# Kernel optimization log

Measured on AMD Instinct MI355X. Metric: run time of the kernel, lower is better.

Reference implementation:

```python
import jax, jax.numpy as jnp
import numpy as np

N_HEADS = 4

def log_cosh(x):
    # numerically stable log(cosh(x)) = |x| + log1p(exp(-2|x|)) - log(2)
    ax = jnp.abs(x)
    return ax + jnp.log1p(jnp.exp(-2.0 * ax)) - jnp.log(2.0)

def setup_inputs() -> dict:
    key = jax.random.key(0)
    ks = jax.random.split(key, 7)
    B, I, A, E, H = 4, 2048, 2048, 256, N_HEADS
    return {
        "query": jax.random.normal(ks[0], (B, I, E), dtype=jnp.float32),
        "key": jax.random.normal(ks[1], (B, A, E), dtype=jnp.float32),
        "value": jax.random.normal(ks[2], (B, A, E), dtype=jnp.float32),
        "distances": jax.random.uniform(ks[3], (B, I, A), dtype=jnp.float32),
        "in_proj_w": jax.random.normal(ks[4], (3 * E, E), dtype=jnp.float32) * 0.05,
        "out_proj_w": jax.random.normal(ks[5], (E, E), dtype=jnp.float32) * 0.05,
        "mass_w": jax.random.normal(ks[6], (H, E), dtype=jnp.float32) * 0.05,
    }

def reference(query, key, value, distances, in_proj_w, out_proj_w, mass_w):
    B, I, E = query.shape
    A = key.shape[1]
    H = N_HEADS
    D = E // H
    # distance-decay additive bias: mass is (B, A, H), nonnegative via log_cosh
    mass = log_cosh(key @ mass_w.T)                       # (B, A, H)
    bias = jnp.einsum('bah,bia->bhia', -mass, distances)  # (B, H, I, A)
    # nn.MultiheadAttention (bias=False) projections
    wq, wk, wv = jnp.split(in_proj_w, 3, axis=0)          # each (E, E)
    q = (query @ wq.T).reshape(B, I, H, D).transpose(0, 2, 1, 3)  # (B,H,I,D)
    k = (key @ wk.T).reshape(B, A, H, D).transpose(0, 2, 1, 3)    # (B,H,A,D)
    v = (value @ wv.T).reshape(B, A, H, D).transpose(0, 2, 1, 3)  # (B,H,A,D)
    scale = 1.0 / jnp.sqrt(jnp.asarray(D, dtype=q.dtype))
    scores = jnp.einsum('bhid,bhad->bhia', q, k) * scale + bias
    attn = jax.nn.softmax(scores, axis=-1)
    o = jnp.einsum('bhia,bhad->bhid', attn, v)            # (B,H,I,D)
    o = o.transpose(0, 2, 1, 3).reshape(B, I, E)
    return o @ out_proj_w.T
```

## Files before the change

kernel.cpp:

```cpp
#include <hip/hip_runtime.h>
#include <hip/hip_bf16.h>
#include <math.h>

#define BB 4
#define II 2048
#define AA 2048
#define EE 256
#define HH 4

#define LOG2E 1.4426950408889634f
#define SCL   (0.125f * LOG2E)

typedef __bf16 bf16_t;
typedef bf16_t bf16x8 __attribute__((ext_vector_type(8)));
typedef bf16_t bf16x4 __attribute__((ext_vector_type(4)));
typedef float  f32x4  __attribute__((ext_vector_type(4)));

static __device__ __forceinline__ f32x4 mfma16(bf16x8 a, bf16x8 b, f32x4 c) {
    return __builtin_amdgcn_mfma_f32_16x16x32_bf16(a, b, c, 0, 0, 0);
}

static __device__ __forceinline__ void glds16(const bf16_t* g, const bf16_t* l) {
    __builtin_amdgcn_global_load_lds(
        (const __attribute__((address_space(1))) void*)g,
        (__attribute__((address_space(3))) void*)l, 16, 0, 0);
}

static __device__ __forceinline__ void proj_body(
    const float* __restrict__ Aop, const float* __restrict__ Bop,
    bf16_t* __restrict__ Cout, int m0, int n0, int TRANS, float cscale,
    bf16_t (*sA)[72], bf16_t (*sB)[72])
{
    const int t = threadIdx.x;
    const int w = t >> 6, l = t & 63, g = l >> 4, q = l & 15;
    const int wm = w >> 1, wn = w & 1;
    const int r = t >> 2, s = t & 3;

    f32x4 acc[2][2] = {};

    for (int kt = 0; kt < 4; ++kt) {
        {
            const float* ga = Aop + (size_t)(m0 + r) * EE + kt * 64 + s * 16;
            float tmp[16];
            *(f32x4*)&tmp[0]  = *(const f32x4*)(ga + 0);
            *(f32x4*)&tmp[4]  = *(const f32x4*)(ga + 4);
            *(f32x4*)&tmp[8]  = *(const f32x4*)(ga + 8);
            *(f32x4*)&tmp[12] = *(const f32x4*)(ga + 12);
            bf16x8 w0, w1;
            #pragma unroll
            for (int i = 0; i < 8; ++i) { w0[i] = (bf16_t)tmp[i]; w1[i] = (bf16_t)tmp[8 + i]; }
            *(bf16x8*)&sA[r][s * 16]     = w0;
            *(bf16x8*)&sA[r][s * 16 + 8] = w1;
        }
        {
            const float* gb = Bop + (size_t)(n0 + r) * EE + kt * 64 + s * 16;
            float tmp[16];
            *(f32x4*)&tmp[0]  = *(const f32x4*)(gb + 0);
            *(f32x4*)&tmp[4]  = *(const f32x4*)(gb + 4);
            *(f32x4*)&tmp[8]  = *(const f32x4*)(gb + 8);
            *(f32x4*)&tmp[12] = *(const f32x4*)(gb + 12);
            bf16x8 w0, w1;
            #pragma unroll
            for (int i = 0; i < 8; ++i) { w0[i] = (bf16_t)tmp[i]; w1[i] = (bf16_t)tmp[8 + i]; }
            *(bf16x8*)&sB[r][s * 16]     = w0;
            *(bf16x8*)&sB[r][s * 16 + 8] = w1;
        }
        __syncthreads();
        #pragma unroll
        for (int ks = 0; ks < 2; ++ks) {
            bf16x8 aA[2], aB[2];
            #pragma unroll
            for (int f = 0; f < 2; ++f) {
                aA[f] = *(const bf16x8*)&sA[wm * 32 + f * 16 + q][ks * 32 + g * 8];
                aB[f] = *(const bf16x8*)&sB[wn * 32 + f * 16 + q][ks * 32 + g * 8];
            }
            #pragma unroll
            for (int fm = 0; fm < 2; ++fm)
            #pragma unroll
            for (int fn = 0; fn < 2; ++fn)
                acc[fm][fn] = mfma16(aA[fm], aB[fn], acc[fm][fn]);
        }
        __syncthreads();
    }
    #pragma unroll
    for (int fm = 0; fm < 2; ++fm)
    #pragma unroll
    for (int fn = 0; fn < 2; ++fn)
    #pragma unroll
    for (int j = 0; j < 4; ++j) {
        const int m = m0 + wm * 32 + fm * 16 + g * 4 + j;
        const int n = n0 + wn * 32 + fn * 16 + q;
        const bf16_t v = (bf16_t)(acc[fm][fn][j] * cscale);
        if (TRANS == 0) {
            Cout[(size_t)m * EE + n] = v;
        } else {
            const int bb = n >> 11, a = n & (AA - 1);
            const int a6 = a & 63;
            const int p6 = (a6 & 32) | ((a6 & 12) << 1) | ((a6 & 16) >> 2) | (a6 & 3);
            Cout[(size_t)bb * (AA * EE) + (size_t)(a >> 6) * (EE * 64) + m * 64 + p6] = v;
        }
    }
}

__global__ __launch_bounds__(256) void fused_pre(
    const float* __restrict__ query, const float* __restrict__ key,
    const float* __restrict__ value, const float* __restrict__ in_w,
    const float* __restrict__ mass_w,
    bf16_t* __restrict__ Qp, bf16_t* __restrict__ Kp, bf16_t* __restrict__ Vt,
    float* __restrict__ massT)
{
    __shared__ __align__(16) bf16_t sA[64][72];
    __shared__ __align__(16) bf16_t sB[64][72];
    const int z = blockIdx.z;
    if (z == 0) {
        proj_body(query, in_w, Qp, blockIdx.x * 64, blockIdx.y * 64, 0, SCL, sA, sB);
    } else if (z == 1) {
        proj_body(key, in_w + 65536, Kp, blockIdx.x * 64, blockIdx.y * 64, 0, 1.0f, sA, sB);
    } else if (z == 2) {
        proj_body(in_w + 131072, value, Vt, blockIdx.y * 64, blockIdx.x * 64, 1, 1.0f, sA, sB);
    } else {
        const int w = threadIdx.x >> 6, l = threadIdx.x & 63;
        const int p = blockIdx.y * 128 + blockIdx.x;
        const int row0 = p * 16 + w * 4;
        f32x4 mw[HH];
        #pragma unroll
        for (int hh = 0; hh < HH; ++hh)
            mw[hh] = *(const f32x4*)(mass_w + hh * EE + l * 4);
        #pragma unroll
        for (int rr = 0; rr < 4; ++rr) {
            const int row = row0 + rr;
            f32x4 kv = *(const f32x4*)(key + (size_t)row * EE + l * 4);
            f32x4 sd;
            #pragma unroll
            for (int hh = 0; hh < HH; ++hh)
                sd[hh] = kv[0]*mw[hh][0] + kv[1]*mw[hh][1] + kv[2]*mw[hh][2] + kv[3]*mw[hh][3];
            #pragma unroll
            for (int off = 32; off >= 1; off >>= 1) {
                #pragma unroll
                for (int hh = 0; hh < HH; ++hh) sd[hh] += __shfl_xor(sd[hh], off, 64);
            }
            if (l == 0) {
                const int bb = row >> 11, a = row & (AA - 1);
                #pragma unroll
                for (int hh = 0; hh < HH; ++hh) {
                    float ax = fabsf(sd[hh]);
                    massT[((size_t)bb * HH + hh) * AA + a] =
                        (ax + log1pf(__expf(-2.0f * ax)) - 0.693147180559945f) * LOG2E;
                }
            }
        }
    }
}

__global__ __launch_bounds__(256) void out_gemm(
    const bf16_t* __restrict__ Aop, const float* __restrict__ Bop,
    float* __restrict__ Cout)
{
    __shared__ __align__(16) bf16_t sA[64][72];
    __shared__ __align__(16) bf16_t sB[64][72];
    const int t = threadIdx.x;
    const int w = t >> 6, l = t & 63, g = l >> 4, q = l & 15;
    const int wm = w >> 1, wn = w & 1;
    const int m0 = blockIdx.x * 64, n0 = blockIdx.y * 64;
    const int r = t >> 2, s = t & 3;

    f32x4 acc[2][2] = {};

    for (int kt = 0; kt < 4; ++kt) {
        {
            const bf16_t* ga = Aop + (size_t)(m0 + r) * EE + kt * 64 + s * 16;
            *(bf16x8*)&sA[r][s * 16]     = *(const bf16x8*)(ga);
            *(bf16x8*)&sA[r][s * 16 + 8] = *(const bf16x8*)(ga + 8);
        }
        {
            const float* gb = Bop + (size_t)(n0 + r) * EE + kt * 64 + s * 16;
            float tmp[16];
            *(f32x4*)&tmp[0]  = *(const f32x4*)(gb + 0);
            *(f32x4*)&tmp[4]  = *(const f32x4*)(gb + 4);
            *(f32x4*)&tmp[8]  = *(const f32x4*)(gb + 8);
            *(f32x4*)&tmp[12] = *(const f32x4*)(gb + 12);
            bf16x8 w0, w1;
            #pragma unroll
            for (int i = 0; i < 8; ++i) { w0[i] = (bf16_t)tmp[i]; w1[i] = (bf16_t)tmp[8 + i]; }
            *(bf16x8*)&sB[r][s * 16]     = w0;
            *(bf16x8*)&sB[r][s * 16 + 8] = w1;
        }
        __syncthreads();
        #pragma unroll
        for (int ks = 0; ks < 2; ++ks) {
            bf16x8 aA[2], aB[2];
            #pragma unroll
            for (int f = 0; f < 2; ++f) {
                aA[f] = *(const bf16x8*)&sA[wm * 32 + f * 16 + q][ks * 32 + g * 8];
                aB[f] = *(const bf16x8*)&sB[wn * 32 + f * 16 + q][ks * 32 + g * 8];
            }
            #pragma unroll
            for (int fm = 0; fm < 2; ++fm)
            #pragma unroll
            for (int fn = 0; fn < 2; ++fn)
                acc[fm][fn] = mfma16(aA[fm], aB[fn], acc[fm][fn]);
        }
        __syncthreads();
    }
    #pragma unroll
    for (int fm = 0; fm < 2; ++fm)
    #pragma unroll
    for (int fn = 0; fn < 2; ++fn)
    #pragma unroll
    for (int j = 0; j < 4; ++j) {
        const int m = m0 + wm * 32 + fm * 16 + g * 4 + j;
        const int n = n0 + wn * 32 + fn * 16 + q;
        Cout[(size_t)m * EE + n] = acc[fm][fn][j];
    }
}

__global__ __launch_bounds__(512, 4) void attn_kernel(
    const bf16_t* __restrict__ Qp, const bf16_t* __restrict__ Kp,
    const bf16_t* __restrict__ Vt, const float* __restrict__ massT,
    const float* __restrict__ dist, bf16_t* __restrict__ Obuf)
{
    __shared__ __align__(16) bf16_t sK[2][2][4096];
    __shared__ __align__(16) bf16_t sV[2][2][4096];
    __shared__ __align__(16) float  sM[2048];

    const int t = threadIdx.x;
    const int wv = t >> 6, l = t & 63, g = l >> 4, q = l & 15;
    const int s = wv >> 2, rg = wv & 3;
    const int h = blockIdx.y, b = blockIdx.z;
    const int i0 = blockIdx.x * 64;

    *(f32x4*)&sM[t * 4] = *(const f32x4*)(massT + ((size_t)b * HH + h) * AA + t * 4);

    bf16x8 qf[2];
    #pragma unroll
    for (int ks = 0; ks < 2; ++ks)
        qf[ks] = *(const bf16x8*)(Qp + (size_t)(b * II + i0 + rg * 16 + q) * EE
                                     + h * 64 + ks * 32 + g * 8);

    const int u0 = rg * 2;
    const int drow0 = u0 * 8 + (l >> 3);
    const int cs = (l & 7) ^ (drow0 & 7);

    const bf16_t* pkg = Kp + ((size_t)b * AA + s * 64 + drow0) * EE + h * 64 + cs * 8;
    const bf16_t* pvg = Vt + (size_t)b * (AA * EE) + (size_t)s * (EE * 64)
                           + (size_t)(h * 64 + drow0) * 64 + cs * 8;
    const float*  pdg = dist + ((size_t)b * II + i0 + rg * 16 + q) * AA + s * 64 + g * 4;

    auto stage = [&](int kb) {
        #pragma unroll
        for (int u = 0; u < 2; ++u) {
            glds16(pkg + u * (8 * EE), &sK[s][kb][(u0 + u) * 512]);
            glds16(pvg + u * (8 * 64), &sV[s][kb][(u0 + u) * 512]);
        }
    };

    f32x4 rd[2][4];

    stage(0);
    pkg += 128 * EE; pvg += 2 * (EE * 64);
    #pragma unroll
    for (int fa = 0; fa < 4; ++fa) rd[0][fa] = *(const f32x4*)(pdg + fa * 16);
    pdg += 128;
    __syncthreads();

    f32x4 oacc[4] = {};
    f32x4 lacc = {};
    bf16x8 vone;
    #pragma unroll
    for (int j = 0; j < 8; ++j) vone[j] = (bf16_t)1.0f;

    int ma = s * 64;

    #pragma unroll 2
    for (int k = 0; k < 16; ++k) {
        const int kb = k & 1;
        if (k < 15) {
            stage(kb ^ 1);
            pkg += 128 * EE; pvg += 2 * (EE * 64);
            #pragma unroll
            for (int fa = 0; fa < 4; ++fa)
                rd[(k + 1) & 1][fa] = *(const f32x4*)(pdg + fa * 16);
            pdg += 128;
        }

        f32x4 st[4] = {};
        __builtin_amdgcn_s_setprio(1);
        #pragma unroll
        for (int fa = 0; fa < 4; ++fa) {
            const int row = fa * 16 + q;
            #pragma unroll
            for (int ks = 0; ks < 2; ++ks) {
                bf16x8 ak = *(const bf16x8*)&sK[s][kb][row * 64 + (((ks * 4 + g) ^ (row & 7)) * 8)];
                st[fa] = mfma16(ak, qf[ks], st[fa]);
            }
        }
        __builtin_amdgcn_s_setprio(0);

        #pragma unroll
        for (int fa = 0; fa < 4; ++fa) {
            f32x4 ms = *(const f32x4*)&sM[ma + fa * 16 + g * 4];
            #pragma unroll
            for (int j = 0; j < 4; ++j)
                st[fa][j] = exp2f(fmaf(-ms[j], rd[kb][fa][j], st[fa][j]));
        }
        ma += 128;

        bf16x8 pa[2];
        #pragma unroll
        for (int ka = 0; ka < 2; ++ka)
        #pragma unroll
        for (int j = 0; j < 8; ++j)
            pa[ka][j] = (bf16_t)st[2 * ka + (j >> 2)][j & 3];

        __builtin_amdgcn_s_setprio(1);
        #pragma unroll
        for (int ka = 0; ka < 2; ++ka) {
            #pragma unroll
            for (int fd = 0; fd < 4; ++fd) {
                const int row = fd * 16 + q;
                bf16x8 bv = *(const bf16x8*)&sV[s][kb][row * 64 + (((ka * 4 + g) ^ (row & 7)) * 8)];
                oacc[fd] = mfma16(pa[ka], bv, oacc[fd]);
            }
            lacc = mfma16(pa[ka], vone, lacc);
        }
        __builtin_amdgcn_s_setprio(0);

        __syncthreads();
    }

    float* cb = (float*)&sK[0][0][0];
    if (s == 1) {
        float* p = cb + (rg * 64 + l) * 21;
        *(f32x4*)(p) = lacc;
        #pragma unroll
        for (int fd = 0; fd < 4; ++fd) *(f32x4*)(p + 4 + fd * 4) = oacc[fd];
    }
    __syncthreads();
    if (s == 0) {
        const float* p = cb + (rg * 64 + l) * 21;
        const f32x4 lB = *(const f32x4*)(p);
        f32x4 inv;
        #pragma unroll
        for (int j = 0; j < 4; ++j) inv[j] = 1.0f / (lacc[j] + lB[j]);
        #pragma unroll
        for (int fd = 0; fd < 4; ++fd) {
            const f32x4 ob = *(const f32x4*)(p + 4 + fd * 4);
            #pragma unroll
            for (int j = 0; j < 4; ++j) {
                const float o = (oacc[fd][j] + ob[j]) * inv[j];
                Obuf[(size_t)(b * II + i0 + rg * 16 + g * 4 + j) * EE
                     + h * 64 + fd * 16 + q] = (bf16_t)o;
            }
        }
    }
}

extern "C" void kernel_launch(void* const* d_in, const int* in_sizes, int n_in,
                              void* d_out, int out_size, void* d_ws, size_t ws_size,
                              hipStream_t stream)
{
    const float* query  = (const float*)d_in[0];
    const float* key    = (const float*)d_in[1];
    const float* value  = (const float*)d_in[2];
    const float* dist   = (const float*)d_in[3];
    const float* in_w   = (const float*)d_in[4];
    const float* out_w  = (const float*)d_in[5];
    const float* mass_w = (const float*)d_in[6];
    float* out = (float*)d_out;

    char* ws = (char*)d_ws;
    bf16_t* Qp    = (bf16_t*)(ws);
    bf16_t* Kp    = (bf16_t*)(ws + 1 * 4194304);
    bf16_t* Vt    = (bf16_t*)(ws + 2 * 4194304);
    bf16_t* Obuf  = (bf16_t*)(ws + 3 * 4194304);
    float*  massT = (float*) (ws + 4 * 4194304);

    fused_pre<<<dim3(128, 4, 4), dim3(256), 0, stream>>>(
        query, key, value, in_w, mass_w, Qp, Kp, Vt, massT);
    attn_kernel<<<dim3(32, 4, 4), dim3(512), 0, stream>>>(Qp, Kp, Vt, massT, dist, Obuf);
    out_gemm<<<dim3(128, 4), dim3(256), 0, stream>>>(Obuf, out_w, out);
}
```

Before: 80.55 us.

## Split attention key range across four wave groups with two query fragments per wave

Changes the wave decomposition from two key-splits by four row groups into four key-splits by two row groups. Each wave now holds two 16-row query fragments and processes a 32-key slice per step, so each K/V fragment read from shared memory feeds two MFMAs and LDS read traffic per MFMA drops. The V tile layout changes to 32-wide rows without the XOR swizzle. The final reduction now merges partial sums from three wave groups through shared memory. The cost is more accumulator registers per wave and a larger cross-wave combine step.

```diff
diff --git a/kernel.cpp b/kernel.cpp
--- a/kernel.cpp
+++ b/kernel.cpp
@@ -219,57 +219,63 @@
     const bf16_t* __restrict__ Vt, const float* __restrict__ massT,
     const float* __restrict__ dist, bf16_t* __restrict__ Obuf)
 {
-    __shared__ __align__(16) bf16_t sK[2][2][4096];
-    __shared__ __align__(16) bf16_t sV[2][2][4096];
+    __shared__ __align__(16) bf16_t sK[4][2][32 * 64];
+    __shared__ __align__(16) bf16_t sV[4][2][64 * 32];
     __shared__ __align__(16) float  sM[2048];
 
     const int t = threadIdx.x;
     const int wv = t >> 6, l = t & 63, g = l >> 4, q = l & 15;
-    const int s = wv >> 2, rg = wv & 3;
+    const int s = wv >> 1, rg = wv & 1;
     const int h = blockIdx.y, b = blockIdx.z;
     const int i0 = blockIdx.x * 64;
 
     *(f32x4*)&sM[t * 4] = *(const f32x4*)(massT + ((size_t)b * HH + h) * AA + t * 4);
 
-    bf16x8 qf[2];
+    bf16x8 qf[2][2];
+    #pragma unroll
+    for (int fq = 0; fq < 2; ++fq)
     #pragma unroll
     for (int ks = 0; ks < 2; ++ks)
-        qf[ks] = *(const bf16x8*)(Qp + (size_t)(b * II + i0 + rg * 16 + q) * EE
-                                     + h * 64 + ks * 32 + g * 8);
-
-    const int u0 = rg * 2;
-    const int drow0 = u0 * 8 + (l >> 3);
-    const int cs = (l & 7) ^ (drow0 & 7);
-
-    const bf16_t* pkg = Kp + ((size_t)b * AA + s * 64 + drow0) * EE + h * 64 + cs * 8;
-    const bf16_t* pvg = Vt + (size_t)b * (AA * EE) + (size_t)s * (EE * 64)
-                           + (size_t)(h * 64 + drow0) * 64 + cs * 8;
-    const float*  pdg = dist + ((size_t)b * II + i0 + rg * 16 + q) * AA + s * 64 + g * 4;
+        qf[fq][ks] = *(const bf16x8*)(Qp + (size_t)(b * II + i0 + rg * 32 + fq * 16 + q) * EE
+                                         + h * 64 + ks * 32 + g * 8);
+
+    const int kcs = (l & 7) ^ (l >> 3);
+    const bf16_t* pkg = Kp + ((size_t)b * AA + s * 32 + rg * 16 + (l >> 3)) * EE
+                           + h * 64 + kcs * 8;
+
+    const bf16_t* pvg = Vt + (size_t)b * (AA * EE) + (size_t)(s >> 1) * (EE * 64)
+                           + (size_t)(h * 64 + rg * 32 + (l >> 2)) * 64
+                           + (s & 1) * 32 + (l & 3) * 8;
+
+    const float* pdg0 = dist + ((size_t)(b * II + i0 + rg * 32 + q)) * AA + s * 32 + g * 4;
+    const float* pdg1 = pdg0 + (size_t)16 * AA;
 
     auto stage = [&](int kb) {
-        #pragma unroll
-        for (int u = 0; u < 2; ++u) {
-            glds16(pkg + u * (8 * EE), &sK[s][kb][(u0 + u) * 512]);
-            glds16(pvg + u * (8 * 64), &sV[s][kb][(u0 + u) * 512]);
-        }
+        glds16(pkg,            &sK[s][kb][(rg * 16) * 64]);
+        glds16(pkg + 8 * EE,   &sK[s][kb][(rg * 16 + 8) * 64]);
+        glds16(pvg,            &sV[s][kb][(rg * 32) * 32]);
+        glds16(pvg + 16 * 64,  &sV[s][kb][(rg * 32 + 16) * 32]);
     };
 
-    f32x4 rd[2][4];
+    f32x4 rd[2][2][2];
 
     stage(0);
     pkg += 128 * EE; pvg += 2 * (EE * 64);
     #pragma unroll
-    for (int fa = 0; fa < 4; ++fa) rd[0][fa] = *(const f32x4*)(pdg + fa * 16);
-    pdg += 128;
+    for (int fa = 0; fa < 2; ++fa) {
+        rd[0][0][fa] = *(const f32x4*)(pdg0 + fa * 16);
+        rd[0][1][fa] = *(const f32x4*)(pdg1 + fa * 16);
+    }
+    pdg0 += 128; pdg1 += 128;
     __syncthreads();
 
-    f32x4 oacc[4] = {};
-    f32x4 lacc = {};
+    f32x4 oacc[2][4] = {};
+    f32x4 lacc[2] = {};
     bf16x8 vone;
     #pragma unroll
     for (int j = 0; j < 8; ++j) vone[j] = (bf16_t)1.0f;
 
-    int ma = s * 64;
+    int ma = s * 32;
 
     #pragma unroll 2
     for (int k = 0; k < 16; ++k) {
@@ -278,78 +284,100 @@
             stage(kb ^ 1);
             pkg += 128 * EE; pvg += 2 * (EE * 64);
             #pragma unroll
-            for (int fa = 0; fa < 4; ++fa)
-                rd[(k + 1) & 1][fa] = *(const f32x4*)(pdg + fa * 16);
-            pdg += 128;
-        }
-
-        f32x4 st[4] = {};
+            for (int fa = 0; fa < 2; ++fa) {
+                rd[kb ^ 1][0][fa] = *(const f32x4*)(pdg0 + fa * 16);
+                rd[kb ^ 1][1][fa] = *(const f32x4*)(pdg1 + fa * 16);
+            }
+            pdg0 += 128; pdg1 += 128;
+        }
+
+        f32x4 st[2][2] = {};
         __builtin_amdgcn_s_setprio(1);
         #pragma unroll
-        for (int fa = 0; fa < 4; ++fa) {
+        for (int fa = 0; fa < 2; ++fa) {
             const int row = fa * 16 + q;
             #pragma unroll
             for (int ks = 0; ks < 2; ++ks) {
                 bf16x8 ak = *(const bf16x8*)&sK[s][kb][row * 64 + (((ks * 4 + g) ^ (row & 7)) * 8)];
-                st[fa] = mfma16(ak, qf[ks], st[fa]);
+                st[0][fa] = mfma16(ak, qf[0][ks], st[0][fa]);
+                st[1][fa] = mfma16(ak, qf[1][ks], st[1][fa]);
             }
         }
         __builtin_amdgcn_s_setprio(0);
 
         #pragma unroll
-        for (int fa = 0; fa < 4; ++fa) {
+        for (int fa = 0; fa < 2; ++fa) {
             f32x4 ms = *(const f32x4*)&sM[ma + fa * 16 + g * 4];
             #pragma unroll
+            for (int fq = 0; fq < 2; ++fq)
+            #pragma unroll
             for (int j = 0; j < 4; ++j)
-                st[fa][j] = exp2f(fmaf(-ms[j], rd[kb][fa][j], st[fa][j]));
+                st[fq][fa][j] = exp2f(fmaf(-ms[j], rd[kb][fq][fa][j], st[fq][fa][j]));
         }
         ma += 128;
 
         bf16x8 pa[2];
         #pragma unroll
-        for (int ka = 0; ka < 2; ++ka)
+        for (int fq = 0; fq < 2; ++fq)
         #pragma unroll
         for (int j = 0; j < 8; ++j)
-            pa[ka][j] = (bf16_t)st[2 * ka + (j >> 2)][j & 3];
+            pa[fq][j] = (bf16_t)st[fq][j >> 2][j & 3];
 
         __builtin_amdgcn_s_setprio(1);
         #pragma unroll
-        for (int ka = 0; ka < 2; ++ka) {
-            #pragma unroll
-            for (int fd = 0; fd < 4; ++fd) {
-                const int row = fd * 16 + q;
-                bf16x8 bv = *(const bf16x8*)&sV[s][kb][row * 64 + (((ka * 4 + g) ^ (row & 7)) * 8)];
-                oacc[fd] = mfma16(pa[ka], bv, oacc[fd]);
-            }
-            lacc = mfma16(pa[ka], vone, lacc);
-        }
+        for (int fd = 0; fd < 4; ++fd) {
+            const int row = fd * 16 + q;
+            bf16x8 bv = *(const bf16x8*)&sV[s][kb][row * 32 + g * 8];
+            oacc[0][fd] = mfma16(pa[0], bv, oacc[0][fd]);
+            oacc[1][fd] = mfma16(pa[1], bv, oacc[1][fd]);
+        }
+        lacc[0] = mfma16(pa[0], vone, lacc[0]);
+        lacc[1] = mfma16(pa[1], vone, lacc[1]);
         __builtin_amdgcn_s_setprio(0);
 
         __syncthreads();
     }
 
     float* cb = (float*)&sK[0][0][0];
-    if (s == 1) {
-        float* p = cb + (rg * 64 + l) * 21;
-        *(f32x4*)(p) = lacc;
-        #pragma unroll
-        for (int fd = 0; fd < 4; ++fd) *(f32x4*)(p + 4 + fd * 4) = oacc[fd];
+    if (s > 0) {
+        float* p = cb + (((s - 1) * 2 + rg) * 64 + l) * 41;
+        *(f32x4*)(p)     = lacc[0];
+        *(f32x4*)(p + 4) = lacc[1];
+        #pragma unroll
+        for (int fq = 0; fq < 2; ++fq)
+        #pragma unroll
+        for (int fd = 0; fd < 4; ++fd)
+            *(f32x4*)(p + 8 + (fq * 4 + fd) * 4) = oacc[fq][fd];
     }
     __syncthreads();
     if (s == 0) {
-        const float* p = cb + (rg * 64 + l) * 21;
-        const f32x4 lB = *(const f32x4*)(p);
-        f32x4 inv;
-        #pragma unroll
-        for (int j = 0; j < 4; ++j) inv[j] = 1.0f / (lacc[j] + lB[j]);
-        #pragma unroll
-        for (int fd = 0; fd < 4; ++fd) {
-            const f32x4 ob = *(const f32x4*)(p + 4 + fd * 4);
+        #pragma unroll
+        for (int u = 0; u < 3; ++u) {
+            const float* p = cb + ((u * 2 + rg) * 64 + l) * 41;
+            const f32x4 l0 = *(const f32x4*)(p);
+            const f32x4 l1 = *(const f32x4*)(p + 4);
+            #pragma unroll
+            for (int j = 0; j < 4; ++j) { lacc[0][j] += l0[j]; lacc[1][j] += l1[j]; }
+            #pragma unroll
+            for (int fq = 0; fq < 2; ++fq)
+            #pragma unroll
+            for (int fd = 0; fd < 4; ++fd) {
+                const f32x4 ob = *(const f32x4*)(p + 8 + (fq * 4 + fd) * 4);
+                #pragma unroll
+                for (int j = 0; j < 4; ++j) oacc[fq][fd][j] += ob[j];
+            }
+        }
+        #pragma unroll
+        for (int fq = 0; fq < 2; ++fq) {
+            f32x4 inv;
+            #pragma unroll
+            for (int j = 0; j < 4; ++j) inv[j] = 1.0f / lacc[fq][j];
+            #pragma unroll
+            for (int fd = 0; fd < 4; ++fd)
             #pragma unroll
             for (int j = 0; j < 4; ++j) {
-                const float o = (oacc[fd][j] + ob[j]) * inv[j];
-                Obuf[(size_t)(b * II + i0 + rg * 16 + g * 4 + j) * EE
-                     + h * 64 + fd * 16 + q] = (bf16_t)o;
+                Obuf[(size_t)(b * II + i0 + rg * 32 + fq * 16 + g * 4 + j) * EE
+                     + h * 64 + fd * 16 + q] = (bf16_t)(oacc[fq][fd][j] * inv[j]);
             }
         }
     }
```

Result: slower. 107.7 us (+33.7%).
